# Kernel optimization log

Hardware: AMD Instinct MI355X
Metric: run time of the kernel (lower is better)

## Reference

```python
import jax, jax.numpy as jnp
import numpy as np

N = 200_000      # num_nodes
D = 32           # embedding_dim
E = 6_400_000    # num edges (avg degree 32)
L = 3            # num_layers


def setup_inputs() -> dict:
    key = jax.random.key(0)
    k1, k2, k3, k4 = jax.random.split(key, 4)
    # xavier_uniform init: bound = sqrt(6 / (fan_in + fan_out))
    bound = float(np.sqrt(6.0 / (N + D)))
    embedding = jax.random.uniform(k1, (N, D), minval=-bound, maxval=bound, dtype=jnp.float32)
    row_idx = jax.random.randint(k2, (E,), 0, N, dtype=jnp.int32)
    col_idx = jax.random.randint(k3, (E,), 0, N, dtype=jnp.int32)
    # normalized adjacency values (roughly 1/degree scale, like sym-normalized LightGCN adj)
    vals = jax.random.uniform(k4, (E,), minval=0.0, maxval=2.0 / 32.0, dtype=jnp.float32)
    return {"embedding": embedding, "vals": vals, "row_idx": row_idx,
            "col_idx": col_idx, "num_layers": L}


def reference(embedding, vals, row_idx, col_idx, num_layers):
    # LightGCN propagation: e^{l+1} = A @ e^{l} (sparse COO SpMM via gather + scatter-add),
    # output = mean over layer outputs [e^0, e^1, ..., e^L].
    n = embedding.shape[0]
    e = embedding
    acc = embedding  # running sum of layer outputs (fused, avoids stacking)
    for _ in range(num_layers):
        msgs = vals[:, None] * e[col_idx]                      # [E, D] gather + scale
        e = jax.ops.segment_sum(msgs, row_idx, num_segments=n)  # [N, D] scatter-add
        acc = acc + e
    return acc / jnp.asarray(num_layers + 1, dtype=embedding.dtype)
```

## Files before the change

### kernel.cpp

```cpp
#include <hip/hip_runtime.h>
#include <hip/hip_bf16.h>
#include <hip/hip_fp16.h>

#define DIM 32
#define BSHIFT 8
#define BROWS 256
#define CAP 12288
#define CHUNK 8192
#define KMAX 1024


__global__ void lgcn_bhist(const int* __restrict__ row,
                           int* __restrict__ bcount, int E, int K) {
    __shared__ int h[KMAX];
    int t = threadIdx.x;
    for (int b = t; b < K; b += blockDim.x) h[b] = 0;
    __syncthreads();
    for (int i = blockIdx.x * blockDim.x + t; i < E; i += gridDim.x * blockDim.x)
        atomicAdd(&h[row[i] >> BSHIFT], 1);
    __syncthreads();
    for (int b = t; b < K; b += blockDim.x)
        if (h[b]) atomicAdd(&bcount[b], h[b]);
}

__global__ void lgcn_bscan(const int* __restrict__ bcount,
                           int* __restrict__ bbase, int* __restrict__ bcursor, int K) {
    __shared__ int s[1024];
    int t = threadIdx.x;
    int v = (t < K) ? bcount[t] : 0;
    s[t] = v;
    __syncthreads();
    for (int off = 1; off < 1024; off <<= 1) {
        int u = (t >= off) ? s[t - off] : 0;
        __syncthreads();
        s[t] += u;
        __syncthreads();
    }
    if (t < K) {
        int excl = s[t] - v;
        bbase[t] = excl;
        bcursor[t] = excl;
    }
    if (t == 0) bbase[K] = s[1023];
}

__launch_bounds__(1024)
__global__ void lgcn_bin(const int* __restrict__ row, const int* __restrict__ col,
                         const float* __restrict__ vals, int* __restrict__ bcursor,
                         int2* __restrict__ binned, int E, int K) {
    __shared__ int hh[KMAX];
    __shared__ int lb[KMAX + 1];
    __shared__ int cur[KMAX];
    __shared__ int2 sbuf[CHUNK];
    int t = threadIdx.x;
    int base = blockIdx.x * CHUNK;
    int cnt = E - base;
    if (cnt > CHUNK) cnt = CHUNK;

    for (int b = t; b < K; b += 1024) hh[b] = 0;
    __syncthreads();

    int  myb[CHUNK / 1024];
    int2 mycv[CHUNK / 1024];
    for (int k = 0; k < CHUNK / 1024; ++k) {
        int i = base + k * 1024 + t;
        if (i < base + cnt) {
            int r = row[i];
            myb[k] = r >> BSHIFT;
            mycv[k] = make_int2(col[i] | ((r & (BROWS - 1)) << 24),
                                __float_as_int(vals[i]));
            atomicAdd(&hh[myb[k]], 1);
        } else myb[k] = -1;
    }
    __syncthreads();

    int v = (t < K) ? hh[t] : 0;
    lb[t] = v;
    __syncthreads();
    for (int off = 1; off < 1024; off <<= 1) {
        int u = (t >= off) ? lb[t - off] : 0;
        __syncthreads();
        lb[t] += u;
        __syncthreads();
    }
    if (t == 0) lb[K] = cnt;
    int excl = lb[t] - v;
    __syncthreads();
    if (t < K) {
        lb[t] = excl;
        cur[t] = excl;
        int gbase = v ? atomicAdd(&bcursor[t], v) : 0;
        hh[t] = gbase - excl;
    }
    __syncthreads();

    for (int k = 0; k < CHUNK / 1024; ++k) {
        if (myb[k] >= 0) {
            int pos = atomicAdd(&cur[myb[k]], 1);
            sbuf[pos] = mycv[k];
        }
    }
    __syncthreads();

    for (int p = t; p < cnt; p += 1024) {
        int lo = 0, hi = K;
        while (hi - lo > 1) {
            int mid = (lo + hi) >> 1;
            if (lb[mid] <= p) lo = mid; else hi = mid;
        }
        binned[hh[lo] + p] = sbuf[p];
    }
}

__global__ void lgcn_bsort(const int* __restrict__ bbase,
                           int2* __restrict__ perm,
                           int* __restrict__ row_end, int N) {
    __shared__ int2 sorted[CAP];
    __shared__ int cnt[BROWS], scn[BROWS], cur[BROWS];
    int b = blockIdx.x, t = threadIdx.x;
    int sB = bbase[b], eB = bbase[b + 1];
    int nB = eB - sB;
    if (t < BROWS) cnt[t] = 0;
    __syncthreads();
    for (int i = sB + t; i < eB; i += 1024)
        atomicAdd(&cnt[(unsigned)perm[i].x >> 24], 1);
    __syncthreads();
    if (t < BROWS) scn[t] = cnt[t];
    __syncthreads();
    for (int off = 1; off < BROWS; off <<= 1) {
        int u = (t >= off && t < BROWS) ? scn[t - off] : 0;
        __syncthreads();
        if (t < BROWS) scn[t] += u;
        __syncthreads();
    }
    int g0 = b << BSHIFT;
    if (t < BROWS) {
        if (g0 + t < N) row_end[g0 + t] = sB + scn[t];
        cur[t] = scn[t] - cnt[t];
    }
    __syncthreads();
    for (int i = sB + t; i < eB; i += 1024) {
        int2 cv = perm[i];
        int r = (unsigned)cv.x >> 24;
        int p = atomicAdd(&cur[r], 1);
        if (p < CAP) sorted[p] = cv;
    }
    __syncthreads();
    for (int p = t; p < nB; p += 1024) {
        int pp = p < CAP ? p : CAP - 1;
        int2 cv = sorted[pp];
        perm[sB + p] = make_int2(cv.x & 0x00FFFFFF, cv.y);
    }
}

__global__ void lgcn_f2h(const float* __restrict__ src,
                         __half2* __restrict__ dst, int n2) {
    int i = blockIdx.x * blockDim.x + threadIdx.x;
    if (i >= n2) return;
    float2 v = ((const float2*)src)[i];
    dst[i] = __float22half2_rn(v);
}

template <int MODE>
__global__ void lgcn_pull(const int* __restrict__ row_end,
                          const int2* __restrict__ perm,
                          const __half2* __restrict__ e_cur,
                          __half2* __restrict__ e_next,
                          const float* __restrict__ emb,
                          float* __restrict__ out, int N) {
    int g = blockIdx.x * (blockDim.x >> 5) + (threadIdx.x >> 5);
    if (g >= N) return;
    int l = threadIdx.x & 31;
    int sub = l >> 4;
    int d2 = l & 15;
    int beg = (g == 0) ? 0 : row_end[g - 1];
    int end = row_end[g];
    float ax = 0.f, ay = 0.f;
    int p = beg + sub;
    for (; p + 6 < end; p += 8) {
        int2 c0 = perm[p];
        int2 c1 = perm[p + 2];
        int2 c2 = perm[p + 4];
        int2 c3 = perm[p + 6];
        float2 x0 = __half22float2(e_cur[(size_t)c0.x * 16 + d2]);
        float2 x1 = __half22float2(e_cur[(size_t)c1.x * 16 + d2]);
        float2 x2 = __half22float2(e_cur[(size_t)c2.x * 16 + d2]);
        float2 x3 = __half22float2(e_cur[(size_t)c3.x * 16 + d2]);
        float v0 = __int_as_float(c0.y), v1 = __int_as_float(c1.y);
        float v2 = __int_as_float(c2.y), v3 = __int_as_float(c3.y);
        ax = fmaf(v0, x0.x, ax); ay = fmaf(v0, x0.y, ay);
        ax = fmaf(v1, x1.x, ax); ay = fmaf(v1, x1.y, ay);
        ax = fmaf(v2, x2.x, ax); ay = fmaf(v2, x2.y, ay);
        ax = fmaf(v3, x3.x, ax); ay = fmaf(v3, x3.y, ay);
    }
    for (; p < end; p += 2) {
        int2 cv = perm[p];
        float2 x = __half22float2(e_cur[(size_t)cv.x * 16 + d2]);
        float v = __int_as_float(cv.y);
        ax = fmaf(v, x.x, ax); ay = fmaf(v, x.y, ay);
    }
    ax += __shfl_xor(ax, 16);
    ay += __shfl_xor(ay, 16);
    if (sub == 0) {
        size_t o2 = (size_t)g * 16 + d2;
        if (MODE == 0) {
            e_next[o2] = __float22half2_rn(make_float2(ax, ay));
            float2 e0 = ((const float2*)emb)[o2];
            ((float2*)out)[o2] = make_float2(e0.x + ax, e0.y + ay);
        } else if (MODE == 1) {
            e_next[o2] = __float22half2_rn(make_float2(ax, ay));
            float2 c = ((float2*)out)[o2];
            ((float2*)out)[o2] = make_float2(c.x + ax, c.y + ay);
        } else {
            float2 c = ((float2*)out)[o2];
            ((float2*)out)[o2] = make_float2((c.x + ax) * 0.25f,
                                             (c.y + ay) * 0.25f);
        }
    }
}


__global__ void lgcn_scatter(const float* __restrict__ e_cur,
                             float* __restrict__ e_next,
                             const float* __restrict__ vals,
                             const int* __restrict__ row_idx,
                             const int* __restrict__ col_idx, int E) {
    int g = blockIdx.x * (blockDim.x >> 5) + (threadIdx.x >> 5);
    if (g >= E) return;
    int d = threadIdx.x & 31;
    int c = col_idx[g];
    int r = row_idx[g];
    float v = vals[g];
    atomicAdd(&e_next[(size_t)r * DIM + d], v * e_cur[(size_t)c * DIM + d]);
}

__global__ void lgcn_add_init(const float* __restrict__ a, const float* __restrict__ b,
                              float* __restrict__ out, int n4) {
    int i = blockIdx.x * blockDim.x + threadIdx.x;
    if (i >= n4) return;
    float4 x = ((const float4*)a)[i]; float4 y = ((const float4*)b)[i];
    ((float4*)out)[i] = make_float4(x.x + y.x, x.y + y.y, x.z + y.z, x.w + y.w);
}
__global__ void lgcn_add(const float* __restrict__ b, float* __restrict__ out, int n4) {
    int i = blockIdx.x * blockDim.x + threadIdx.x;
    if (i >= n4) return;
    float4 x = ((float4*)out)[i]; float4 y = ((const float4*)b)[i];
    ((float4*)out)[i] = make_float4(x.x + y.x, x.y + y.y, x.z + y.z, x.w + y.w);
}
__global__ void lgcn_add_scale(const float* __restrict__ b, float* __restrict__ out,
                               int n4, float s) {
    int i = blockIdx.x * blockDim.x + threadIdx.x;
    if (i >= n4) return;
    float4 x = ((float4*)out)[i]; float4 y = ((const float4*)b)[i];
    ((float4*)out)[i] = make_float4((x.x + y.x) * s, (x.y + y.y) * s,
                                    (x.z + y.z) * s, (x.w + y.w) * s);
}

extern "C" void kernel_launch(void* const* d_in, const int* in_sizes, int n_in,
                              void* d_out, int out_size, void* d_ws, size_t ws_size,
                              hipStream_t stream) {
    const float* emb  = (const float*)d_in[0];
    const float* vals = (const float*)d_in[1];
    const int*   row  = (const int*)d_in[2];
    const int*   col  = (const int*)d_in[3];

    const int N = in_sizes[0] / DIM;
    const int E = in_sizes[1];
    float* out  = (float*)d_out;

    const int K = (N + BROWS - 1) >> BSHIFT;

    const size_t hwords = (size_t)N * DIM / 2;
    __half2* emb_h  = (__half2*)d_ws;
    __half2* bufA_h = (__half2*)((int*)d_ws + hwords);
    __half2* bufB_h = (__half2*)((int*)d_ws + 2 * hwords);
    int*   row_end = (int*)d_ws + 3 * hwords;
    int*   bcount  = row_end + N;
    int*   bbase   = bcount + K;
    int*   bcursor = bbase + (K + 1);
    size_t word_off = (size_t)((bcursor + K) - (int*)d_ws);
    word_off = (word_off + 1) & ~(size_t)1;
    int2*  perm    = (int2*)((int*)d_ws + word_off);
    const size_t needed = (word_off + (size_t)2 * E) * 4;

    const int n4 = N * DIM / 4;
    const int n2 = N * DIM / 2;
    const int add_grid = (n4 + 255) / 256;
    const size_t layer_bytes = (size_t)N * DIM * sizeof(float);

    const double mean_bucket = (double)E / (double)N * BROWS;
    const bool csr_ok = (ws_size >= needed) && (K <= KMAX) &&
                        (mean_bucket * 1.45 < (double)CAP) &&
                        (N < (1 << 24)) && (DIM % 4 == 0);

    if (!csr_ok) {
        float* bufA = (float*)d_ws;
        float* bufB = bufA + (size_t)N * DIM;
        const int sct_grid = (E + 7) / 8;
        hipMemsetAsync(bufA, 0, layer_bytes, stream);
        lgcn_scatter<<<sct_grid, 256, 0, stream>>>(emb, bufA, vals, row, col, E);
        lgcn_add_init<<<add_grid, 256, 0, stream>>>(emb, bufA, out, n4);
        hipMemsetAsync(bufB, 0, layer_bytes, stream);
        lgcn_scatter<<<sct_grid, 256, 0, stream>>>(bufA, bufB, vals, row, col, E);
        lgcn_add<<<add_grid, 256, 0, stream>>>(bufB, out, n4);
        hipMemsetAsync(bufA, 0, layer_bytes, stream);
        lgcn_scatter<<<sct_grid, 256, 0, stream>>>(bufB, bufA, vals, row, col, E);
        lgcn_add_scale<<<add_grid, 256, 0, stream>>>(bufA, out, n4, 0.25f);
        return;
    }

    const int bin_grid = (E + CHUNK - 1) / CHUNK;
    hipMemsetAsync(bcount, 0, (size_t)K * sizeof(int), stream);
    lgcn_f2h<<<(n2 + 255) / 256, 256, 0, stream>>>(emb, emb_h, n2);
    lgcn_bhist<<<bin_grid, 256, 0, stream>>>(row, bcount, E, K);
    lgcn_bscan<<<1, 1024, 0, stream>>>(bcount, bbase, bcursor, K);
    lgcn_bin<<<bin_grid, 1024, 0, stream>>>(row, col, vals, bcursor, perm, E, K);
    lgcn_bsort<<<K, 1024, 0, stream>>>(bbase, perm, row_end, N);

    const int pull_grid = (N + 7) / 8;
    lgcn_pull<0><<<pull_grid, 256, 0, stream>>>(row_end, perm, emb_h, bufA_h, emb, out, N);
    lgcn_pull<1><<<pull_grid, 256, 0, stream>>>(row_end, perm, bufA_h, bufB_h, emb, out, N);
    lgcn_pull<2><<<pull_grid, 256, 0, stream>>>(row_end, perm, bufB_h, nullptr, emb, out, N);
}
```

Before: 457.1 us.

## Split CSR into int column and fp16 value arrays, add nontemporal loads

New measurement: 536.5 us. 1.17x slower.

```diff
diff --git a/kernel.cpp b/kernel.cpp
--- a/kernel.cpp
+++ b/kernel.cpp
@@ -9,6 +9,19 @@
 #define CHUNK 8192
 #define KMAX 1024
 
+template <typename T>
+__device__ __forceinline__ T ntload(const T* p) { return __builtin_nontemporal_load(p); }
+
+__device__ __forceinline__ float h2f_bits(unsigned short w) {
+    __half_raw hr;
+    hr.x = w;
+    return __half2float(__half(hr));
+}
+__device__ __forceinline__ unsigned short f2h_bits(float f) {
+    __half_raw hr = __half_raw(__float2half(f));
+    return hr.x;
+}
+
 
 __global__ void lgcn_bhist(const int* __restrict__ row,
                            int* __restrict__ bcount, int E, int K) {
@@ -17,7 +30,7 @@
     for (int b = t; b < K; b += blockDim.x) h[b] = 0;
     __syncthreads();
     for (int i = blockIdx.x * blockDim.x + t; i < E; i += gridDim.x * blockDim.x)
-        atomicAdd(&h[row[i] >> BSHIFT], 1);
+        atomicAdd(&h[ntload(row + i) >> BSHIFT], 1);
     __syncthreads();
     for (int b = t; b < K; b += blockDim.x)
         if (h[b]) atomicAdd(&bcount[b], h[b]);
@@ -47,11 +60,13 @@
 __launch_bounds__(1024)
 __global__ void lgcn_bin(const int* __restrict__ row, const int* __restrict__ col,
                          const float* __restrict__ vals, int* __restrict__ bcursor,
-                         int2* __restrict__ binned, int E, int K) {
+                         int* __restrict__ bcr, unsigned short* __restrict__ bvh,
+                         int E, int K) {
     __shared__ int hh[KMAX];
     __shared__ int lb[KMAX + 1];
     __shared__ int cur[KMAX];
-    __shared__ int2 sbuf[CHUNK];
+    __shared__ int sbuf_cr[CHUNK];
+    __shared__ unsigned short sbuf_vh[CHUNK];
     int t = threadIdx.x;
     int base = blockIdx.x * CHUNK;
     int cnt = E - base;
@@ -60,15 +75,16 @@
     for (int b = t; b < K; b += 1024) hh[b] = 0;
     __syncthreads();
 
-    int  myb[CHUNK / 1024];
-    int2 mycv[CHUNK / 1024];
+    int            myb[CHUNK / 1024];
+    int            mycr[CHUNK / 1024];
+    unsigned short myvh[CHUNK / 1024];
     for (int k = 0; k < CHUNK / 1024; ++k) {
         int i = base + k * 1024 + t;
         if (i < base + cnt) {
-            int r = row[i];
+            int r = ntload(row + i);
             myb[k] = r >> BSHIFT;
-            mycv[k] = make_int2(col[i] | ((r & (BROWS - 1)) << 24),
-                                __float_as_int(vals[i]));
+            mycr[k] = ntload(col + i) | ((r & (BROWS - 1)) << 24);
+            myvh[k] = f2h_bits(ntload(vals + i));
             atomicAdd(&hh[myb[k]], 1);
         } else myb[k] = -1;
     }
@@ -97,7 +113,8 @@
     for (int k = 0; k < CHUNK / 1024; ++k) {
         if (myb[k] >= 0) {
             int pos = atomicAdd(&cur[myb[k]], 1);
-            sbuf[pos] = mycv[k];
+            sbuf_cr[pos] = mycr[k];
+            sbuf_vh[pos] = myvh[k];
         }
     }
     __syncthreads();
@@ -108,14 +125,17 @@
             int mid = (lo + hi) >> 1;
             if (lb[mid] <= p) lo = mid; else hi = mid;
         }
-        binned[hh[lo] + p] = sbuf[p];
+        int g = hh[lo] + p;
+        bcr[g] = sbuf_cr[p];
+        bvh[g] = sbuf_vh[p];
     }
 }
 
 __global__ void lgcn_bsort(const int* __restrict__ bbase,
-                           int2* __restrict__ perm,
+                           int* __restrict__ bcr, unsigned short* __restrict__ bvh,
                            int* __restrict__ row_end, int N) {
-    __shared__ int2 sorted[CAP];
+    __shared__ int sorted_cr[CAP];
+    __shared__ unsigned short sorted_vh[CAP];
     __shared__ int cnt[BROWS], scn[BROWS], cur[BROWS];
     int b = blockIdx.x, t = threadIdx.x;
     int sB = bbase[b], eB = bbase[b + 1];
@@ -123,7 +143,7 @@
     if (t < BROWS) cnt[t] = 0;
     __syncthreads();
     for (int i = sB + t; i < eB; i += 1024)
-        atomicAdd(&cnt[(unsigned)perm[i].x >> 24], 1);
+        atomicAdd(&cnt[(unsigned)ntload(bcr + i) >> 24], 1);
     __syncthreads();
     if (t < BROWS) scn[t] = cnt[t];
     __syncthreads();
@@ -140,16 +160,17 @@
     }
     __syncthreads();
     for (int i = sB + t; i < eB; i += 1024) {
-        int2 cv = perm[i];
-        int r = (unsigned)cv.x >> 24;
+        int cr = bcr[i];
+        unsigned short vh = bvh[i];
+        int r = (unsigned)cr >> 24;
         int p = atomicAdd(&cur[r], 1);
-        if (p < CAP) sorted[p] = cv;
+        if (p < CAP) { sorted_cr[p] = cr; sorted_vh[p] = vh; }
     }
     __syncthreads();
     for (int p = t; p < nB; p += 1024) {
         int pp = p < CAP ? p : CAP - 1;
-        int2 cv = sorted[pp];
-        perm[sB + p] = make_int2(cv.x & 0x00FFFFFF, cv.y);
+        bcr[sB + p] = sorted_cr[pp] & 0x00FFFFFF;
+        bvh[sB + p] = sorted_vh[pp];
     }
 }
 
@@ -163,7 +184,8 @@
 
 template <int MODE>
 __global__ void lgcn_pull(const int* __restrict__ row_end,
-                          const int2* __restrict__ perm,
+                          const int* __restrict__ cols,
+                          const unsigned short* __restrict__ vh,
                           const __half2* __restrict__ e_cur,
                           __half2* __restrict__ e_next,
                           const float* __restrict__ emb,
@@ -178,25 +200,32 @@
     float ax = 0.f, ay = 0.f;
     int p = beg + sub;
     for (; p + 6 < end; p += 8) {
-        int2 c0 = perm[p];
-        int2 c1 = perm[p + 2];
-        int2 c2 = perm[p + 4];
-        int2 c3 = perm[p + 6];
-        float2 x0 = __half22float2(e_cur[(size_t)c0.x * 16 + d2]);
-        float2 x1 = __half22float2(e_cur[(size_t)c1.x * 16 + d2]);
-        float2 x2 = __half22float2(e_cur[(size_t)c2.x * 16 + d2]);
-        float2 x3 = __half22float2(e_cur[(size_t)c3.x * 16 + d2]);
-        float v0 = __int_as_float(c0.y), v1 = __int_as_float(c1.y);
-        float v2 = __int_as_float(c2.y), v3 = __int_as_float(c3.y);
+        int c0 = ntload(cols + p);
+        int c1 = ntload(cols + p + 2);
+        int c2 = ntload(cols + p + 4);
+        int c3 = ntload(cols + p + 6);
+        unsigned short w0 = ntload(vh + p);
+        unsigned short w1 = ntload(vh + p + 2);
+        unsigned short w2 = ntload(vh + p + 4);
+        unsigned short w3 = ntload(vh + p + 6);
+        float2 x0 = __half22float2(e_cur[(size_t)c0 * 16 + d2]);
+        float2 x1 = __half22float2(e_cur[(size_t)c1 * 16 + d2]);
+        float2 x2 = __half22float2(e_cur[(size_t)c2 * 16 + d2]);
+        float2 x3 = __half22float2(e_cur[(size_t)c3 * 16 + d2]);
+        float v0 = h2f_bits(w0);
+        float v1 = h2f_bits(w1);
+        float v2 = h2f_bits(w2);
+        float v3 = h2f_bits(w3);
         ax = fmaf(v0, x0.x, ax); ay = fmaf(v0, x0.y, ay);
         ax = fmaf(v1, x1.x, ax); ay = fmaf(v1, x1.y, ay);
         ax = fmaf(v2, x2.x, ax); ay = fmaf(v2, x2.y, ay);
         ax = fmaf(v3, x3.x, ax); ay = fmaf(v3, x3.y, ay);
     }
     for (; p < end; p += 2) {
-        int2 cv = perm[p];
-        float2 x = __half22float2(e_cur[(size_t)cv.x * 16 + d2]);
-        float v = __int_as_float(cv.y);
+        int c = ntload(cols + p);
+        unsigned short w = ntload(vh + p);
+        float2 x = __half22float2(e_cur[(size_t)c * 16 + d2]);
+        float v = h2f_bits(w);
         ax = fmaf(v, x.x, ax); ay = fmaf(v, x.y, ay);
     }
     ax += __shfl_xor(ax, 16);
@@ -278,10 +307,9 @@
     int*   bcount  = row_end + N;
     int*   bbase   = bcount + K;
     int*   bcursor = bbase + (K + 1);
-    size_t word_off = (size_t)((bcursor + K) - (int*)d_ws);
-    word_off = (word_off + 1) & ~(size_t)1;
-    int2*  perm    = (int2*)((int*)d_ws + word_off);
-    const size_t needed = (word_off + (size_t)2 * E) * 4;
+    int*   colsbuf = bcursor + K;
+    unsigned short* vhbuf = (unsigned short*)(colsbuf + E);
+    const size_t needed = ((size_t)(colsbuf - (int*)d_ws) + (size_t)E + (E + 1) / 2) * 4;
 
     const int n4 = N * DIM / 4;
     const int n2 = N * DIM / 2;
@@ -291,7 +319,7 @@
     const double mean_bucket = (double)E / (double)N * BROWS;
     const bool csr_ok = (ws_size >= needed) && (K <= KMAX) &&
                         (mean_bucket * 1.45 < (double)CAP) &&
-                        (N < (1 << 24)) && (DIM % 4 == 0);
+                        (N < (1 << 24)) && (DIM == 32);
 
     if (!csr_ok) {
         float* bufA = (float*)d_ws;
@@ -314,11 +342,15 @@
     lgcn_f2h<<<(n2 + 255) / 256, 256, 0, stream>>>(emb, emb_h, n2);
     lgcn_bhist<<<bin_grid, 256, 0, stream>>>(row, bcount, E, K);
     lgcn_bscan<<<1, 1024, 0, stream>>>(bcount, bbase, bcursor, K);
-    lgcn_bin<<<bin_grid, 1024, 0, stream>>>(row, col, vals, bcursor, perm, E, K);
-    lgcn_bsort<<<K, 1024, 0, stream>>>(bbase, perm, row_end, N);
+    lgcn_bin<<<bin_grid, 1024, 0, stream>>>(row, col, vals, bcursor,
+                                            colsbuf, vhbuf, E, K);
+    lgcn_bsort<<<K, 1024, 0, stream>>>(bbase, colsbuf, vhbuf, row_end, N);
 
     const int pull_grid = (N + 7) / 8;
-    lgcn_pull<0><<<pull_grid, 256, 0, stream>>>(row_end, perm, emb_h, bufA_h, emb, out, N);
-    lgcn_pull<1><<<pull_grid, 256, 0, stream>>>(row_end, perm, bufA_h, bufB_h, emb, out, N);
-    lgcn_pull<2><<<pull_grid, 256, 0, stream>>>(row_end, perm, bufB_h, nullptr, emb, out, N);
-}
+    lgcn_pull<0><<<pull_grid, 256, 0, stream>>>(row_end, colsbuf, vhbuf,
+                                                emb_h, bufA_h, emb, out, N);
+    lgcn_pull<1><<<pull_grid, 256, 0, stream>>>(row_end, colsbuf, vhbuf,
+                                                bufA_h, bufB_h, emb, out, N);
+    lgcn_pull<2><<<pull_grid, 256, 0, stream>>>(row_end, colsbuf, vhbuf,
+                                                bufB_h, nullptr, emb, out, N);
+}
```
